# Kernel tuning notes

Measured on AMD Instinct MI355X. Metric: run time of the kernel, lower is better.

The kernel has to match this reference:

```python
import jax, jax.numpy as jnp
import numpy as np
from jax import lax

B, T, D_IN, D_PROJ, D_OUT, LORDER = 16, 2048, 1024, 512, 1024, 20


def setup_inputs() -> dict:
    key = jax.random.key(0)
    k1, k2, k3, k4 = jax.random.split(key, 4)
    s = 0.05
    return {
        "input": jax.random.normal(k1, (B, T, D_IN), dtype=jnp.float32),
        "in_cache": jnp.zeros((B, D_PROJ, LORDER - 1), dtype=jnp.float32),
        "W_lin": jax.random.normal(k2, (D_IN, D_PROJ), dtype=jnp.float32) * s,
        "conv_w": jax.random.normal(k3, (D_PROJ, LORDER), dtype=jnp.float32) * s,
        "W_aff": jax.random.normal(k4, (D_PROJ, D_OUT), dtype=jnp.float32) * s,
        "b_aff": jnp.zeros((D_OUT,), dtype=jnp.float32),
    }


def reference(input, in_cache, W_lin, conv_w, W_aff, b_aff):
    L = conv_w.shape[1]
    # 1) linear down-projection (no bias): [B,T,Din] -> [B,T,Dp]
    x = jnp.einsum("btd,dp->btp", input, W_lin)
    # 2) FSMN causal depthwise memory block with streaming cache
    xt = jnp.swapaxes(x, 1, 2)                       # [B,Dp,T]
    cat = jnp.concatenate([in_cache, xt], axis=2)    # [B,Dp,T+L-1]
    out_cache = cat[:, :, -(L - 1):]                 # last L-1 frames for next chunk
    # depthwise conv over time, VALID padding -> output length T
    y = lax.conv_general_dilated(
        cat, conv_w[:, None, :],                      # rhs [Dp,1,L]
        window_strides=(1,), padding="VALID",
        dimension_numbers=("NCH", "OIH", "NCH"),
        feature_group_count=conv_w.shape[0])
    m = jnp.swapaxes(y + xt, 1, 2)                   # residual add, back to [B,T,Dp]
    # 3) affine up-projection + 4) ReLU
    out = jax.nn.relu(jnp.einsum("btp,po->bto", m, W_aff) + b_aff)
    return (out, out_cache)
```

## Files before the change

kernel.cpp:

```cpp
#include <hip/hip_runtime.h>
#include <cstdint>
#include <cstddef>

#define B_  16
#define T_  2048
#define DIN 1024
#define DPJ 512
#define DOUT 1024
#define LORD 20
#define HALO (LORD - 1)
#define M_ROWS (B_ * T_)
#define OUT0_ELEMS ((size_t)M_ROWS * DOUT)
#define CACHE_ELEMS ((size_t)B_ * DPJ * (LORD - 1))

typedef __bf16 bf16_t;
typedef __bf16 bf16x2 __attribute__((ext_vector_type(2)));
typedef __bf16 bf16x4 __attribute__((ext_vector_type(4)));
typedef __bf16 bf16x8 __attribute__((ext_vector_type(8)));
typedef float  f32x4  __attribute__((ext_vector_type(4)));

__device__ __forceinline__ void async_load16(const void* g, void* lds_base) {
    __builtin_amdgcn_global_load_lds(
        (const __attribute__((address_space(1))) unsigned int*)g,
        (__attribute__((address_space(3))) unsigned int*)lds_base,
        16, 0, 0);
}

__device__ __forceinline__ int xcd_swizzle(int hw, int nwg) {
    int cpx = nwg >> 3;
    return (hw & 7) * cpx + (hw >> 3);
}

__global__ __launch_bounds__(256) void prep_weights(
    const float* __restrict__ Wl, const float* __restrict__ Wa,
    bf16_t* __restrict__ WlT, bf16_t* __restrict__ WaT) {
    int idx = blockIdx.x * 256 + threadIdx.x;
    const int n1 = DIN * DPJ;
    if (idx < n1) {
        int n = idx >> 10;
        int k = idx - (n << 10);
        WlT[idx] = (bf16_t)Wl[(size_t)k * DPJ + n];
    } else {
        int j = idx - n1;
        if (j < DPJ * DOUT) {
            int n = j >> 9;
            int k = j - (n << 9);
            WaT[j] = (bf16_t)Wa[(size_t)k * DOUT + n];
        }
    }
}

#define XR 160
#define PADC 136
__global__ __launch_bounds__(512, 4) void gemm1_conv(
    const float* __restrict__ A, const bf16_t* __restrict__ Bt,
    const float* __restrict__ cache, const float* __restrict__ cw,
    bf16_t* __restrict__ m, float* __restrict__ oc) {
    __shared__ __align__(16) char ldsraw[73728];
    bf16_t* sA0 = (bf16_t*)(ldsraw);
    bf16_t* sA1 = (bf16_t*)(ldsraw + 20480);
    bf16_t* sB0 = (bf16_t*)(ldsraw + 40960);
    bf16_t* sB1 = (bf16_t*)(ldsraw + 57344);
    bf16_t* xb  = (bf16_t*)(ldsraw);

    const int tid  = threadIdx.x;
    const int lane = tid & 63;
    const int wave = tid >> 6;
    const int K    = DIN;

    const int gx   = gridDim.x;
    const int hw   = blockIdx.y * gx + blockIdx.x;
    const int lid  = xcd_swizzle(hw, gx * gridDim.y);
    const int lby  = lid / gx;
    const int lbx  = lid - lby * gx;
    const int col0 = lbx * 128;
    const int b    = lby >> 4;
    const int tloc = (lby & 15) * 128;
    const float* Ab = A + (size_t)b * T_ * DIN;

    size_t aoff[5];
    int    doff[5];
#pragma unroll
    for (int i = 0; i < 5; ++i) {
        int u = tid + 512 * i;
        int r = u >> 4, c16 = u & 15;
        int t = tloc - 32 + r; if (t < 0) t = 0;
        aoff[i] = (size_t)t * DIN + c16 * 4;
        doff[i] = r * 64 + (((c16 >> 1) ^ (r & 7)) << 3) + (c16 & 1) * 4;
    }

    const int lr  = lane >> 3;
    const int jsw = (lane & 7) ^ lr;
    const bf16_t* gB0 = Bt + (size_t)(col0 + wave * 16 + lr) * K + jsw * 8;

    const int wm = (wave >> 2) * 80;
    const int wn = (wave & 3) * 32;
    const int fr = lane & 15;
    const int fk = lane >> 4;

    const f32x4 zero = {0.f, 0.f, 0.f, 0.f};
    f32x4 acc[5][2];
#pragma unroll
    for (int mt = 0; mt < 5; ++mt)
#pragma unroll
        for (int nt = 0; nt < 2; ++nt) acc[mt][nt] = zero;

    f32x4 P[5];
    auto load_a = [&](int kk) {
#pragma unroll
        for (int i = 0; i < 5; ++i) P[i] = *(const f32x4*)(Ab + aoff[i] + kk);
    };
    auto cvt_write = [&](bf16_t* dst) {
#pragma unroll
        for (int i = 0; i < 5; ++i) {
            bf16x4 v = { (bf16_t)P[i][0], (bf16_t)P[i][1],
                         (bf16_t)P[i][2], (bf16_t)P[i][3] };
            *(bf16x4*)(dst + doff[i]) = v;
        }
    };
    auto stage_b = [&](int kk, bf16_t* dstB) {
#pragma unroll
        for (int c = 0; c < 2; ++c)
            async_load16(gB0 + (size_t)c * 8 * K + kk, dstB + wave * 1024 + c * 512);
    };
    auto compute = [&](const bf16_t* bA, const bf16_t* bB) {
#pragma unroll
        for (int h = 0; h < 2; ++h) {
            bf16x8 af[5], bfr[2];
#pragma unroll
            for (int mt = 0; mt < 5; ++mt) {
                int r = wm + mt * 16 + fr;
                int j = h * 4 + fk;
                af[mt] = *(const bf16x8*)(bA + r * 64 + ((j ^ (r & 7)) << 3));
            }
#pragma unroll
            for (int nt = 0; nt < 2; ++nt) {
                int r = wn + nt * 16 + fr;
                int j = h * 4 + fk;
                bfr[nt] = *(const bf16x8*)(bB + r * 64 + ((j ^ (r & 7)) << 3));
            }
#pragma unroll
            for (int mt = 0; mt < 5; ++mt)
#pragma unroll
                for (int nt = 0; nt < 2; ++nt)
                    acc[mt][nt] = __builtin_amdgcn_mfma_f32_16x16x32_bf16(
                        af[mt], bfr[nt], acc[mt][nt], 0, 0, 0);
        }
    };

    load_a(0);
    stage_b(0, sB0);
    cvt_write(sA0);
    load_a(64);

    for (int k0 = 0; k0 < K; k0 += 128) {
        asm volatile("s_waitcnt vmcnt(5) lgkmcnt(0)" ::: "memory");
        __builtin_amdgcn_sched_barrier(0);
        __builtin_amdgcn_s_barrier();
        __builtin_amdgcn_sched_barrier(0);
        stage_b(k0 + 64, sB1);
        cvt_write(sA1);
        if (k0 + 128 < K) load_a(k0 + 128);
        compute(sA0, sB0);

        if (k0 + 128 < K) {
            asm volatile("s_waitcnt vmcnt(5) lgkmcnt(0)" ::: "memory");
        } else {
            asm volatile("s_waitcnt vmcnt(0) lgkmcnt(0)" ::: "memory");
        }
        __builtin_amdgcn_sched_barrier(0);
        __builtin_amdgcn_s_barrier();
        __builtin_amdgcn_sched_barrier(0);
        if (k0 + 128 < K) {
            stage_b(k0 + 128, sB0);
            cvt_write(sA0);
            if (k0 + 192 < K) load_a(k0 + 192);
        }
        compute(sA1, sB1);
    }

    __syncthreads();
    {
        const int er_l = wm + (lane >> 4) * 4;
        const int ec_l = wn + (lane & 15);
#pragma unroll
        for (int mt = 0; mt < 5; ++mt)
#pragma unroll
            for (int nt = 0; nt < 2; ++nt)
#pragma unroll
                for (int rr = 0; rr < 4; ++rr)
                    xb[(er_l + mt * 16 + rr) * PADC + ec_l + nt * 16] =
                        (bf16_t)acc[mt][nt][rr];
    }
    __syncthreads();

    if (tloc == 0) {
        for (int i2 = tid; i2 < HALO * 128; i2 += 512) {
            int rr2 = i2 >> 7;
            int cc  = i2 & 127;
            xb[(13 + rr2) * PADC + cc] =
                (bf16_t)cache[((size_t)b * DPJ + col0 + cc) * HALO + rr2];
        }
    }
    __syncthreads();

    {
        const int pp   = tid & 63;
        const int tb   = (tid >> 6) * 16;
        const int pg_l = 2 * pp;
        const int pg   = col0 + pg_l;

        float2 w[LORD];
#pragma unroll
        for (int l = 0; l < LORD; ++l) {
            w[l].x = cw[pg * LORD + l];
            w[l].y = cw[(pg + 1) * LORD + l];
        }
        auto rdx = [&](int r) -> float2 {
            bf16x2 v = *(const bf16x2*)(xb + r * PADC + pg_l);
            float2 f; f.x = (float)v[0]; f.y = (float)v[1]; return f;
        };
        float2 win[LORD];
#pragma unroll
        for (int i = 0; i < HALO; ++i) win[i] = rdx(tb + 13 + i);
#pragma unroll
        for (int tl = 0; tl < 16; ++tl) {
            float2 nv = rdx(tb + 13 + tl + HALO);
            win[(tl + HALO) % LORD] = nv;
            float2 s = nv;
#pragma unroll
            for (int l = 0; l < LORD; ++l) {
                float2 v = win[(tl + l) % LORD];
                s.x += w[l].x * v.x;
                s.y += w[l].y * v.y;
            }
            bf16x2 o = { (bf16_t)s.x, (bf16_t)s.y };
            *(bf16x2*)(m + ((size_t)(b * T_ + tloc + tb + tl)) * DPJ + pg) = o;
        }
    }

    if (tloc == T_ - 128) {
        for (int i2 = tid; i2 < 128 * HALO; i2 += 512) {
            int pl = i2 / HALO;
            int j  = i2 - pl * HALO;
            oc[((size_t)b * DPJ + col0 + pl) * HALO + j] =
                (float)xb[(141 + j) * PADC + pl];
        }
    }
}

__global__ __launch_bounds__(256) void gemm_bt_relu(
    const bf16_t* __restrict__ A, const bf16_t* __restrict__ Bt,
    float* __restrict__ C, const float* __restrict__ bias,
    const int M, const int N, const int K) {
    __shared__ bf16_t sA[2][128 * 64];
    __shared__ bf16_t sB[2][128 * 64];

    const int tid  = threadIdx.x;
    const int lane = tid & 63;
    const int wave = tid >> 6;

    const int gx   = gridDim.x;
    const int hw   = blockIdx.y * gx + blockIdx.x;
    const int lid  = xcd_swizzle(hw, gx * gridDim.y);
    const int lby  = lid / gx;
    const int lbx  = lid - lby * gx;
    const int col0 = lbx * 128;
    const int row0 = lby * 128;

    const int lr   = lane >> 3;
    const int jsw  = (lane & 7) ^ lr;
    const bf16_t* gA0 = A  + (size_t)(row0 + wave * 32 + lr) * K + jsw * 8;
    const bf16_t* gB0 = Bt + (size_t)(col0 + wave * 32 + lr) * K + jsw * 8;

    const int wm = (wave >> 1) * 64;
    const int wn = (wave & 1) * 64;
    const int fr = lane & 15;
    const int fk = lane >> 4;

    const f32x4 zero = {0.f, 0.f, 0.f, 0.f};
    f32x4 acc[4][4];
#pragma unroll
    for (int mt = 0; mt < 4; ++mt)
#pragma unroll
        for (int nt = 0; nt < 4; ++nt) acc[mt][nt] = zero;

    auto stage = [&](int kk, bf16_t* dA, bf16_t* dB) {
#pragma unroll
        for (int c = 0; c < 4; ++c) {
            async_load16(gA0 + (size_t)c * 8 * K + kk, dA + wave * 2048 + c * 512);
            async_load16(gB0 + (size_t)c * 8 * K + kk, dB + wave * 2048 + c * 512);
        }
    };
    auto compute = [&](const bf16_t* bA, const bf16_t* bB) {
#pragma unroll
        for (int h = 0; h < 2; ++h) {
            bf16x8 af[4], bfr[4];
#pragma unroll
            for (int mt = 0; mt < 4; ++mt) {
                int r = wm + mt * 16 + fr;
                int j = h * 4 + fk;
                af[mt] = *(const bf16x8*)(bA + r * 64 + ((j ^ (r & 7)) << 3));
            }
#pragma unroll
            for (int nt = 0; nt < 4; ++nt) {
                int r = wn + nt * 16 + fr;
                int j = h * 4 + fk;
                bfr[nt] = *(const bf16x8*)(bB + r * 64 + ((j ^ (r & 7)) << 3));
            }
#pragma unroll
            for (int mt = 0; mt < 4; ++mt)
#pragma unroll
                for (int nt = 0; nt < 4; ++nt)
                    acc[mt][nt] = __builtin_amdgcn_mfma_f32_16x16x32_bf16(
                        af[mt], bfr[nt], acc[mt][nt], 0, 0, 0);
        }
    };

    stage(0, sA[0], sB[0]);

    for (int k0 = 0; k0 < K; k0 += 128) {
        asm volatile("s_waitcnt vmcnt(0)" ::: "memory");
        __builtin_amdgcn_sched_barrier(0);
        __builtin_amdgcn_s_barrier();
        __builtin_amdgcn_sched_barrier(0);
        stage(k0 + 64, sA[1], sB[1]);
        compute(sA[0], sB[0]);

        asm volatile("s_waitcnt vmcnt(0)" ::: "memory");
        __builtin_amdgcn_sched_barrier(0);
        __builtin_amdgcn_s_barrier();
        __builtin_amdgcn_sched_barrier(0);
        const int kn2 = k0 + 128;
        if (kn2 < K) stage(kn2, sA[0], sB[0]);
        compute(sA[1], sB[1]);
    }

    const int er = row0 + wm + (lane >> 4) * 4;
    const int ec = col0 + wn + (lane & 15);
#pragma unroll
    for (int nt = 0; nt < 4; ++nt) {
        float bb = bias[ec + nt * 16];
#pragma unroll
        for (int mt = 0; mt < 4; ++mt)
#pragma unroll
            for (int rr = 0; rr < 4; ++rr) {
                float v = acc[mt][nt][rr] + bb;
                C[(size_t)(er + mt * 16 + rr) * N + (ec + nt * 16)] =
                    v > 0.f ? v : 0.f;
            }
    }
}

extern "C" void kernel_launch(void* const* d_in, const int* in_sizes, int n_in,
                              void* d_out, int out_size, void* d_ws, size_t ws_size,
                              hipStream_t stream) {
    const float* input    = (const float*)d_in[0];
    const float* in_cache = (const float*)d_in[1];
    const float* W_lin    = (const float*)d_in[2];
    const float* conv_w   = (const float*)d_in[3];
    const float* W_aff    = (const float*)d_in[4];
    const float* b_aff    = (const float*)d_in[5];
    float* out = (float*)d_out;

    char* ws = (char*)d_ws;
    bf16_t* m_buf = (bf16_t*)(ws + 33554432);
    bf16_t* WlinT = (bf16_t*)(ws + 67108864);
    bf16_t* WaffT = (bf16_t*)(ws + 67108864 + 1048576);

    prep_weights<<<(DIN * DPJ + DPJ * DOUT + 255) / 256, 256, 0, stream>>>(
        W_lin, W_aff, WlinT, WaffT);

    gemm1_conv<<<dim3(DPJ / 128, M_ROWS / 128), 512, 0, stream>>>(
        input, WlinT, in_cache, conv_w, m_buf, out + OUT0_ELEMS);

    gemm_bt_relu<<<dim3(DOUT / 128, M_ROWS / 128), 256, 0, stream>>>(
        m_buf, WaffT, out, b_aff, M_ROWS, DOUT, DPJ);
}
```

Measured before the change: 332.7 us.

## Fuse weight transpose/convert into GEMM B-tile loads, drop prep kernel

Removes the separate prep_weights kernel that transposed and converted both weight matrices to bf16. Each GEMM now reads fp32 weights directly with strided scalar loads, converts them in registers and writes them to swizzled LDS. This saves one launch and a weight round-trip through memory. In exchange every block repeats the conversion, the B loads are scalar (though coalesced across threads), and more barriers are added per k-step.

```diff
diff --git a/kernel.cpp b/kernel.cpp
--- a/kernel.cpp
+++ b/kernel.cpp
@@ -11,7 +11,6 @@
 #define HALO (LORD - 1)
 #define M_ROWS (B_ * T_)
 #define OUT0_ELEMS ((size_t)M_ROWS * DOUT)
-#define CACHE_ELEMS ((size_t)B_ * DPJ * (LORD - 1))
 
 typedef __bf16 bf16_t;
 typedef __bf16 bf16x2 __attribute__((ext_vector_type(2)));
@@ -19,6 +18,8 @@
 typedef __bf16 bf16x8 __attribute__((ext_vector_type(8)));
 typedef float  f32x4  __attribute__((ext_vector_type(4)));
 
+#define SBAR __builtin_amdgcn_sched_barrier(0)
+
 __device__ __forceinline__ void async_load16(const void* g, void* lds_base) {
     __builtin_amdgcn_global_load_lds(
         (const __attribute__((address_space(1))) unsigned int*)g,
@@ -31,29 +32,10 @@
     return (hw & 7) * cpx + (hw >> 3);
 }
 
-__global__ __launch_bounds__(256) void prep_weights(
-    const float* __restrict__ Wl, const float* __restrict__ Wa,
-    bf16_t* __restrict__ WlT, bf16_t* __restrict__ WaT) {
-    int idx = blockIdx.x * 256 + threadIdx.x;
-    const int n1 = DIN * DPJ;
-    if (idx < n1) {
-        int n = idx >> 10;
-        int k = idx - (n << 10);
-        WlT[idx] = (bf16_t)Wl[(size_t)k * DPJ + n];
-    } else {
-        int j = idx - n1;
-        if (j < DPJ * DOUT) {
-            int n = j >> 9;
-            int k = j - (n << 9);
-            WaT[j] = (bf16_t)Wa[(size_t)k * DOUT + n];
-        }
-    }
-}
-
 #define XR 160
 #define PADC 136
 __global__ __launch_bounds__(512, 4) void gemm1_conv(
-    const float* __restrict__ A, const bf16_t* __restrict__ Bt,
+    const float* __restrict__ A, const float* __restrict__ Wl,
     const float* __restrict__ cache, const float* __restrict__ cw,
     bf16_t* __restrict__ m, float* __restrict__ oc) {
     __shared__ __align__(16) char ldsraw[73728];
@@ -89,9 +71,11 @@
         doff[i] = r * 64 + (((c16 >> 1) ^ (r & 7)) << 3) + (c16 & 1) * 4;
     }
 
-    const int lr  = lane >> 3;
-    const int jsw = (lane & 7) ^ lr;
-    const bf16_t* gB0 = Bt + (size_t)(col0 + wave * 16 + lr) * K + jsw * 8;
+    const int bn  = tid >> 2;
+    const int bkg = (tid & 3) * 2;
+    const float* gW = Wl + (size_t)(bkg * 8) * DPJ + col0 + bn;
+    const int bo0 = bn * 64 + ((bkg       ^ (bn & 7)) << 3);
+    const int bo1 = bn * 64 + (((bkg + 1) ^ (bn & 7)) << 3);
 
     const int wm = (wave >> 2) * 80;
     const int wn = (wave & 3) * 32;
@@ -106,11 +90,16 @@
         for (int nt = 0; nt < 2; ++nt) acc[mt][nt] = zero;
 
     f32x4 P[5];
+    float bb[16];
     auto load_a = [&](int kk) {
 #pragma unroll
         for (int i = 0; i < 5; ++i) P[i] = *(const f32x4*)(Ab + aoff[i] + kk);
     };
-    auto cvt_write = [&](bf16_t* dst) {
+    auto load_b = [&](int kk) {
+#pragma unroll
+        for (int c = 0; c < 16; ++c) bb[c] = gW[(size_t)(kk + c) * DPJ];
+    };
+    auto cvt_write_a = [&](bf16_t* dst) {
 #pragma unroll
         for (int i = 0; i < 5; ++i) {
             bf16x4 v = { (bf16_t)P[i][0], (bf16_t)P[i][1],
@@ -118,10 +107,13 @@
             *(bf16x4*)(dst + doff[i]) = v;
         }
     };
-    auto stage_b = [&](int kk, bf16_t* dstB) {
-#pragma unroll
-        for (int c = 0; c < 2; ++c)
-            async_load16(gB0 + (size_t)c * 8 * K + kk, dstB + wave * 1024 + c * 512);
+    auto cvt_write_b = [&](bf16_t* dst) {
+        bf16x8 v0 = { (bf16_t)bb[0], (bf16_t)bb[1], (bf16_t)bb[2], (bf16_t)bb[3],
+                      (bf16_t)bb[4], (bf16_t)bb[5], (bf16_t)bb[6], (bf16_t)bb[7] };
+        bf16x8 v1 = { (bf16_t)bb[8],  (bf16_t)bb[9],  (bf16_t)bb[10], (bf16_t)bb[11],
+                      (bf16_t)bb[12], (bf16_t)bb[13], (bf16_t)bb[14], (bf16_t)bb[15] };
+        *(bf16x8*)(dst + bo0) = v0;
+        *(bf16x8*)(dst + bo1) = v1;
     };
     auto compute = [&](const bf16_t* bA, const bf16_t* bB) {
 #pragma unroll
@@ -148,34 +140,28 @@
         }
     };
 
-    load_a(0);
-    stage_b(0, sB0);
-    cvt_write(sA0);
-    load_a(64);
+    load_a(0); load_b(0);
+    cvt_write_a(sA0); cvt_write_b(sB0);
+    load_a(64); load_b(64);
 
     for (int k0 = 0; k0 < K; k0 += 128) {
-        asm volatile("s_waitcnt vmcnt(5) lgkmcnt(0)" ::: "memory");
-        __builtin_amdgcn_sched_barrier(0);
-        __builtin_amdgcn_s_barrier();
-        __builtin_amdgcn_sched_barrier(0);
-        stage_b(k0 + 64, sB1);
-        cvt_write(sA1);
-        if (k0 + 128 < K) load_a(k0 + 128);
+        asm volatile("s_waitcnt lgkmcnt(0)" ::: "memory");
+        SBAR; __builtin_amdgcn_s_barrier(); SBAR;
+        cvt_write_a(sA1);
+        cvt_write_b(sB1);
+        if (k0 + 128 < K) { load_a(k0 + 128); load_b(k0 + 128); }
+        asm volatile("s_waitcnt lgkmcnt(0)" ::: "memory");
+        SBAR; __builtin_amdgcn_s_barrier(); SBAR;
         compute(sA0, sB0);
 
+        asm volatile("s_waitcnt lgkmcnt(0)" ::: "memory");
+        SBAR; __builtin_amdgcn_s_barrier(); SBAR;
         if (k0 + 128 < K) {
-            asm volatile("s_waitcnt vmcnt(5) lgkmcnt(0)" ::: "memory");
-        } else {
-            asm volatile("s_waitcnt vmcnt(0) lgkmcnt(0)" ::: "memory");
-        }
-        __builtin_amdgcn_sched_barrier(0);
-        __builtin_amdgcn_s_barrier();
-        __builtin_amdgcn_sched_barrier(0);
-        if (k0 + 128 < K) {
-            stage_b(k0 + 128, sB0);
-            cvt_write(sA0);
-            if (k0 + 192 < K) load_a(k0 + 192);
-        }
+            cvt_write_a(sA0); cvt_write_b(sB0);
+            if (k0 + 192 < K) { load_a(k0 + 192); load_b(k0 + 192); }
+        }
+        asm volatile("s_waitcnt lgkmcnt(0)" ::: "memory");
+        SBAR; __builtin_amdgcn_s_barrier(); SBAR;
         compute(sA1, sB1);
     }
 
@@ -250,15 +236,16 @@
 }
 
 __global__ __launch_bounds__(256) void gemm_bt_relu(
-    const bf16_t* __restrict__ A, const bf16_t* __restrict__ Bt,
-    float* __restrict__ C, const float* __restrict__ bias,
-    const int M, const int N, const int K) {
+    const bf16_t* __restrict__ A, const float* __restrict__ Wa,
+    float* __restrict__ C, const float* __restrict__ bias) {
     __shared__ bf16_t sA[2][128 * 64];
     __shared__ bf16_t sB[2][128 * 64];
 
     const int tid  = threadIdx.x;
     const int lane = tid & 63;
     const int wave = tid >> 6;
+    const int K    = DPJ;
+    const int N    = DOUT;
 
     const int gx   = gridDim.x;
     const int hw   = blockIdx.y * gx + blockIdx.x;
@@ -270,8 +257,15 @@
 
     const int lr   = lane >> 3;
     const int jsw  = (lane & 7) ^ lr;
-    const bf16_t* gA0 = A  + (size_t)(row0 + wave * 32 + lr) * K + jsw * 8;
-    const bf16_t* gB0 = Bt + (size_t)(col0 + wave * 32 + lr) * K + jsw * 8;
+    const bf16_t* gA0 = A + (size_t)(row0 + wave * 32 + lr) * K + jsw * 8;
+
+    const int bn  = tid >> 1;
+    const int bkg = (tid & 1) * 4;
+    const float* gW = Wa + (size_t)(bkg * 8) * DOUT + col0 + bn;
+    int bo[4];
+#pragma unroll
+    for (int j = 0; j < 4; ++j)
+        bo[j] = bn * 64 + (((bkg + j) ^ (bn & 7)) << 3);
 
     const int wm = (wave >> 1) * 64;
     const int wn = (wave & 1) * 64;
@@ -285,12 +279,24 @@
 #pragma unroll
         for (int nt = 0; nt < 4; ++nt) acc[mt][nt] = zero;
 
-    auto stage = [&](int kk, bf16_t* dA, bf16_t* dB) {
-#pragma unroll
-        for (int c = 0; c < 4; ++c) {
+    float bb[16];
+    auto stage_a = [&](int kk, bf16_t* dA) {
+#pragma unroll
+        for (int c = 0; c < 4; ++c)
             async_load16(gA0 + (size_t)c * 8 * K + kk, dA + wave * 2048 + c * 512);
-            async_load16(gB0 + (size_t)c * 8 * K + kk, dB + wave * 2048 + c * 512);
-        }
+    };
+    auto load_b_half = [&](int kk, int h) {
+#pragma unroll
+        for (int c = 0; c < 16; ++c)
+            bb[c] = gW[(size_t)(kk + h * 16 + c) * DOUT];
+    };
+    auto cvt_write_b_half = [&](bf16_t* dst, int h) {
+        bf16x8 v0 = { (bf16_t)bb[0], (bf16_t)bb[1], (bf16_t)bb[2], (bf16_t)bb[3],
+                      (bf16_t)bb[4], (bf16_t)bb[5], (bf16_t)bb[6], (bf16_t)bb[7] };
+        bf16x8 v1 = { (bf16_t)bb[8],  (bf16_t)bb[9],  (bf16_t)bb[10], (bf16_t)bb[11],
+                      (bf16_t)bb[12], (bf16_t)bb[13], (bf16_t)bb[14], (bf16_t)bb[15] };
+        *(bf16x8*)(dst + bo[h * 2])     = v0;
+        *(bf16x8*)(dst + bo[h * 2 + 1]) = v1;
     };
     auto compute = [&](const bf16_t* bA, const bf16_t* bB) {
 #pragma unroll
@@ -317,22 +323,37 @@
         }
     };
 
-    stage(0, sA[0], sB[0]);
+    stage_a(0, sA[0]);
+    load_b_half(0, 0); cvt_write_b_half(sB[0], 0);
+    load_b_half(0, 1); cvt_write_b_half(sB[0], 1);
 
     for (int k0 = 0; k0 < K; k0 += 128) {
-        asm volatile("s_waitcnt vmcnt(0)" ::: "memory");
-        __builtin_amdgcn_sched_barrier(0);
-        __builtin_amdgcn_s_barrier();
-        __builtin_amdgcn_sched_barrier(0);
-        stage(k0 + 64, sA[1], sB[1]);
+        asm volatile("s_waitcnt lgkmcnt(0)" ::: "memory");
+        SBAR; __builtin_amdgcn_s_barrier(); SBAR;
+        {
+            load_b_half(k0 + 64, 0);
+            cvt_write_b_half(sB[1], 0);
+            load_b_half(k0 + 64, 1);
+            stage_a(k0 + 64, sA[1]);
+            cvt_write_b_half(sB[1], 1);
+        }
+        asm volatile("s_waitcnt lgkmcnt(0)" ::: "memory");
+        SBAR; __builtin_amdgcn_s_barrier(); SBAR;
         compute(sA[0], sB[0]);
 
-        asm volatile("s_waitcnt vmcnt(0)" ::: "memory");
-        __builtin_amdgcn_sched_barrier(0);
-        __builtin_amdgcn_s_barrier();
-        __builtin_amdgcn_sched_barrier(0);
-        const int kn2 = k0 + 128;
-        if (kn2 < K) stage(kn2, sA[0], sB[0]);
+        asm volatile("s_waitcnt lgkmcnt(0)" ::: "memory");
+        SBAR; __builtin_amdgcn_s_barrier(); SBAR;
+        if (k0 + 128 < K) {
+            load_b_half(k0 + 128, 0);
+            cvt_write_b_half(sB[0], 0);
+            load_b_half(k0 + 128, 1);
+            stage_a(k0 + 128, sA[0]);
+            cvt_write_b_half(sB[0], 1);
+        } else {
+            asm volatile("s_waitcnt vmcnt(0)" ::: "memory");
+        }
+        asm volatile("s_waitcnt lgkmcnt(0)" ::: "memory");
+        SBAR; __builtin_amdgcn_s_barrier(); SBAR;
         compute(sA[1], sB[1]);
     }
 
@@ -340,12 +361,12 @@
     const int ec = col0 + wn + (lane & 15);
 #pragma unroll
     for (int nt = 0; nt < 4; ++nt) {
-        float bb = bias[ec + nt * 16];
+        float bbias = bias[ec + nt * 16];
 #pragma unroll
         for (int mt = 0; mt < 4; ++mt)
 #pragma unroll
             for (int rr = 0; rr < 4; ++rr) {
-                float v = acc[mt][nt][rr] + bb;
+                float v = acc[mt][nt][rr] + bbias;
                 C[(size_t)(er + mt * 16 + rr) * N + (ec + nt * 16)] =
                     v > 0.f ? v : 0.f;
             }
@@ -365,15 +386,10 @@
 
     char* ws = (char*)d_ws;
     bf16_t* m_buf = (bf16_t*)(ws + 33554432);
-    bf16_t* WlinT = (bf16_t*)(ws + 67108864);
-    bf16_t* WaffT = (bf16_t*)(ws + 67108864 + 1048576);
-
-    prep_weights<<<(DIN * DPJ + DPJ * DOUT + 255) / 256, 256, 0, stream>>>(
-        W_lin, W_aff, WlinT, WaffT);
 
     gemm1_conv<<<dim3(DPJ / 128, M_ROWS / 128), 512, 0, stream>>>(
-        input, WlinT, in_cache, conv_w, m_buf, out + OUT0_ELEMS);
+        input, W_lin, in_cache, conv_w, m_buf, out + OUT0_ELEMS);
 
     gemm_bt_relu<<<dim3(DOUT / 128, M_ROWS / 128), 256, 0, stream>>>(
-        m_buf, WaffT, out, b_aff, M_ROWS, DOUT, DPJ);
-}
+        m_buf, W_aff, out, b_aff);
+}
```

Result: slower. 452.0 us (+35.9%).
